# Performance work log

Hardware: AMD Instinct MI355X
Metric: run time of the kernel (lower is better)

## Reference

```python
import jax, jax.numpy as jnp
import numpy as np

NUM_NODES = 100000
NUM_EDGES = 600000
NUM_GRAPHS = 512
D = 128  # num_features == latent widths


def setup_inputs() -> dict:
    key = jax.random.key(0)
    ks = jax.random.split(key, 16)
    inp = {
        "x": jax.random.normal(ks[0], (NUM_NODES, D), dtype=jnp.float32),
        "edge_index": jax.random.randint(ks[1], (2, NUM_EDGES), 0, NUM_NODES, dtype=jnp.int32),
        "batch": jnp.sort(jax.random.randint(ks[2], (NUM_NODES,), 0, NUM_GRAPHS, dtype=jnp.int32)),
    }
    s = 1.0 / np.sqrt(D)
    # SAGEConv params per layer: lin_l (applied to mean-aggregated neighbors), lin_r (root), bias
    for i in range(3):
        inp[f"Wl{i+1}"] = jax.random.uniform(ks[3 + 3 * i], (D, D), jnp.float32, -s, s)
        inp[f"Wr{i+1}"] = jax.random.uniform(ks[4 + 3 * i], (D, D), jnp.float32, -s, s)
        inp[f"b{i+1}"] = jax.random.uniform(ks[5 + 3 * i], (D,), jnp.float32, -s, s)
    inp["Wro"] = jax.random.uniform(ks[12], (D, 1), jnp.float32, -s, s)
    inp["bro"] = jax.random.uniform(ks[13], (1,), jnp.float32, -s, s)
    return inp


def _sage_conv(h, Wl, Wr, b, src, dst):
    # mean aggregation of source features at destination nodes
    msg = jax.ops.segment_sum(h[src], dst, num_segments=NUM_NODES)          # [N, D]
    cnt = jax.ops.segment_sum(jnp.ones((src.shape[0], 1), h.dtype), dst,
                              num_segments=NUM_NODES)                        # [N, 1]
    mean = msg / jnp.maximum(cnt, 1.0)
    return mean @ Wl + h @ Wr + b


def reference(x, edge_index, batch, Wl1, Wr1, b1, Wl2, Wr2, b2, Wl3, Wr3, b3, Wro, bro):
    src, dst = edge_index[0], edge_index[1]
    h = x
    for Wl, Wr, b in ((Wl1, Wr1, b1), (Wl2, Wr2, b2), (Wl3, Wr3, b3)):
        h = jax.nn.relu(_sage_conv(h, Wl, Wr, b, src, dst))
    # per-graph sum pooling (replaces the python loop over unique batch ids)
    pooled = jax.ops.segment_sum(h, batch, num_segments=NUM_GRAPHS)  # [G, D]
    return jax.nn.sigmoid(pooled @ Wro + bro)  # [G, 1]
```

## Files before the change

### kernel.cpp

```cpp
#include <hip/hip_runtime.h>
#include <math.h>

#define N_NODES 100000
#define N_EDGES 600000
#define N_GRAPHS 512
#define D 128
#define SCAN_BS 1024
#define SCAN_NBC ((N_NODES + SCAN_BS - 1) / SCAN_BS)
#define NPART 8
#define PART_SZ (N_NODES / NPART)
#define E4 (N_EDGES / 4)
#define SPLIT_B 12500

typedef unsigned short u16;
typedef __attribute__((ext_vector_type(8))) short short8;
typedef __attribute__((ext_vector_type(4))) float f32x4;

__device__ __forceinline__ u16 f2bf(float f) {
    unsigned int u = __float_as_uint(f);
    u += 0x7FFFu + ((u >> 16) & 1u);
    return (u16)(u >> 16);
}
__device__ __forceinline__ float bf2f(u16 h) {
    return __uint_as_float(((unsigned int)h) << 16);
}
__device__ __forceinline__ void split2(float f, unsigned int& h16, unsigned int& l16) {
    unsigned int u = __float_as_uint(f);
    unsigned int hb = (u + (0x7FFFu + ((u >> 16) & 1u))) & 0xffff0000u;
    float lo = f - __uint_as_float(hb);
    unsigned int ul = __float_as_uint(lo);
    h16 = hb >> 16;
    l16 = (ul + (0x7FFFu + ((ul >> 16) & 1u))) >> 16;
}

typedef __attribute__((address_space(1))) const unsigned int gas_u32;
typedef __attribute__((address_space(3))) unsigned int las_u32;
__device__ __forceinline__ void gload16(const void* g, void* l) {
    __builtin_amdgcn_global_load_lds((gas_u32*)g, (las_u32*)l, 16, 0, 0);
}

__global__ __launch_bounds__(256) void zero_i_kernel(int* __restrict__ p, int n) {
    int i = blockIdx.x * 256 + threadIdx.x;
    if (i < n) p[i] = 0;
}

__global__ __launch_bounds__(256) void hist_kernel(const int* __restrict__ dst,
                                                   int* __restrict__ deg) {
    int e = blockIdx.x * 256 + threadIdx.x;
    if (e < N_EDGES) atomicAdd(&deg[dst[e]], 1);
}

__global__ __launch_bounds__(1024) void scan1_kernel(const int* __restrict__ deg,
                                                     int* __restrict__ excl,
                                                     int* __restrict__ blocksum) {
    __shared__ int buf[2][SCAN_BS];
    const int t = threadIdx.x;
    const int gid = blockIdx.x * SCAN_BS + t;
    int v = (gid < N_NODES) ? deg[gid] : 0;
    buf[0][t] = v;
    __syncthreads();
    int pi = 0;
    for (int off = 1; off < SCAN_BS; off <<= 1) {
        int val = buf[pi][t];
        if (t >= off) val += buf[pi][t - off];
        buf[pi ^ 1][t] = val;
        pi ^= 1;
        __syncthreads();
    }
    int incl = buf[pi][t];
    if (gid < N_NODES) excl[gid] = incl - v;
    if (t == SCAN_BS - 1) blocksum[blockIdx.x] = incl;
}

__global__ __launch_bounds__(256) void scan3_kernel(const int* __restrict__ excl,
                                                    const int* __restrict__ blocksum,
                                                    int* __restrict__ rowptr) {
    __shared__ int buf[2][128];
    const int t = threadIdx.x;
    if (t < 128) buf[0][t] = (t < SCAN_NBC) ? blocksum[t] : 0;
    __syncthreads();
    int pi = 0;
    for (int off = 1; off < 128; off <<= 1) {
        if (t < 128) {
            int val = buf[pi][t];
            if (t >= off) val += buf[pi][t - off];
            buf[pi ^ 1][t] = val;
        }
        pi ^= 1;
        __syncthreads();
    }
    const int i = blockIdx.x * 256 + t;
    if (i < N_NODES) {
        const int j = i / SCAN_BS;
        const int pref = (j == 0) ? 0 : buf[pi][j - 1];
        rowptr[i] = excl[i] + pref;
    }
    if (i == 0) rowptr[N_NODES] = N_EDGES;
}

__global__ __launch_bounds__(256) void fill_kernel(const int* __restrict__ src,
                                                   const int* __restrict__ dst,
                                                   const int* __restrict__ rowptr,
                                                   int* __restrict__ fill,
                                                   int* __restrict__ csr_src) {
    const int lo = (blockIdx.x & (NPART - 1)) * PART_SZ;
    const int i4 = (blockIdx.x >> 3) * 256 + threadIdx.x;
    if (i4 >= E4) return;
    const int4 d4 = ((const int4*)dst)[i4];
    const int4 s4 = ((const int4*)src)[i4];
    if ((unsigned)(d4.x - lo) < (unsigned)PART_SZ) {
        int pos = rowptr[d4.x] + atomicAdd(&fill[d4.x], 1);
        csr_src[pos] = s4.x;
    }
    if ((unsigned)(d4.y - lo) < (unsigned)PART_SZ) {
        int pos = rowptr[d4.y] + atomicAdd(&fill[d4.y], 1);
        csr_src[pos] = s4.y;
    }
    if ((unsigned)(d4.z - lo) < (unsigned)PART_SZ) {
        int pos = rowptr[d4.z] + atomicAdd(&fill[d4.z], 1);
        csr_src[pos] = s4.z;
    }
    if ((unsigned)(d4.w - lo) < (unsigned)PART_SZ) {
        int pos = rowptr[d4.w] + atomicAdd(&fill[d4.w], 1);
        csr_src[pos] = s4.w;
    }
}

__global__ __launch_bounds__(256) void prep_kernel(const float* __restrict__ x,
                                                   u16* __restrict__ Hhi,
                                                   u16* __restrict__ Hlo,
                                                   const float* __restrict__ Wl1, const float* __restrict__ Wr1,
                                                   const float* __restrict__ Wl2, const float* __restrict__ Wr2,
                                                   const float* __restrict__ Wl3, const float* __restrict__ Wr3,
                                                   u16* __restrict__ wph, u16* __restrict__ wpl) {
    if (blockIdx.x < SPLIT_B) {
        const int i = blockIdx.x * 256 + threadIdx.x;
        const float4 v = ((const float4*)x)[i];
        unsigned int h0, l0, h1, l1, h2, l2, h3, l3;
        split2(v.x, h0, l0); split2(v.y, h1, l1);
        split2(v.z, h2, l2); split2(v.w, h3, l3);
        uint2 oh, ol;
        oh.x = h0 | (h1 << 16); oh.y = h2 | (h3 << 16);
        ol.x = l0 | (l1 << 16); ol.y = l2 | (l3 << 16);
        ((uint2*)Hhi)[i] = oh;
        ((uint2*)Hlo)[i] = ol;
    } else {
        const int b = (blockIdx.x - SPLIT_B) * 4 + (threadIdx.x >> 6);
        const int lane = threadIdx.x & 63;
        const int layer = b >> 6;
        const int t = b & 63;
        const float* Wl = (layer == 0) ? Wl1 : (layer == 1) ? Wl2 : Wl3;
        const float* Wr = (layer == 0) ? Wr1 : (layer == 1) ? Wr2 : Wr3;
        const int nt = t >> 3, kt = t & 7;
        const int n = nt * 16 + (lane & 15);
        const int k0 = kt * 32 + (lane >> 4) * 8;
        const size_t base = (size_t)layer * 32768 + (size_t)(t * 64 + lane) * 8;
        #pragma unroll
        for (int j = 0; j < 8; ++j) {
            const int k = k0 + j;
            const float w = (k < 128) ? Wl[k * 128 + n] : Wr[(k - 128) * 128 + n];
            const u16 h = f2bf(w);
            wph[base + j] = h;
            wpl[base + j] = f2bf(w - bf2f(h));
        }
    }
}

__global__ __launch_bounds__(256) void agg_kernel(const u16* __restrict__ Hhi,
                                                  const int* __restrict__ rowptr,
                                                  const int* __restrict__ csr_src,
                                                  u16* __restrict__ Mb) {
    const int lane = threadIdx.x & 63;
    const int half = lane >> 5;
    const int q = lane & 31;
    const int node = blockIdx.x * 4 + (threadIdx.x >> 6);
    if (node >= N_NODES) return;
    const int beg = rowptr[node];
    const int end = rowptr[node + 1];
    const uint2* H64 = (const uint2*)Hhi;
    float a0 = 0.f, a1 = 0.f, a2 = 0.f, a3 = 0.f;

    for (int c0 = beg; c0 < end; c0 += 64) {
        const int nv = min(64, end - c0);
        int msrc = (c0 + lane < end) ? csr_src[c0 + lane] : 0;
        int j = 0;
        for (; j + 8 <= nv; j += 8) {
            const int t0 = __shfl(msrc, j + 0 + half);
            const int t1 = __shfl(msrc, j + 2 + half);
            const int t2 = __shfl(msrc, j + 4 + half);
            const int t3 = __shfl(msrc, j + 6 + half);
            const uint2 w0 = H64[(size_t)t0 * 32 + q];
            const uint2 w1 = H64[(size_t)t1 * 32 + q];
            const uint2 w2 = H64[(size_t)t2 * 32 + q];
            const uint2 w3 = H64[(size_t)t3 * 32 + q];
            a0 += __uint_as_float(w0.x << 16) + __uint_as_float(w1.x << 16)
                + __uint_as_float(w2.x << 16) + __uint_as_float(w3.x << 16);
            a1 += __uint_as_float(w0.x & 0xffff0000u) + __uint_as_float(w1.x & 0xffff0000u)
                + __uint_as_float(w2.x & 0xffff0000u) + __uint_as_float(w3.x & 0xffff0000u);
            a2 += __uint_as_float(w0.y << 16) + __uint_as_float(w1.y << 16)
                + __uint_as_float(w2.y << 16) + __uint_as_float(w3.y << 16);
            a3 += __uint_as_float(w0.y & 0xffff0000u) + __uint_as_float(w1.y & 0xffff0000u)
                + __uint_as_float(w2.y & 0xffff0000u) + __uint_as_float(w3.y & 0xffff0000u);
        }
        for (; j + 2 <= nv; j += 2) {
            const int s = __shfl(msrc, j + half);
            const uint2 w = H64[(size_t)s * 32 + q];
            a0 += __uint_as_float(w.x << 16);
            a1 += __uint_as_float(w.x & 0xffff0000u);
            a2 += __uint_as_float(w.y << 16);
            a3 += __uint_as_float(w.y & 0xffff0000u);
        }
        if (j < nv) {
            const int s = __shfl(msrc, j);
            if (half == 0) {
                const uint2 w = H64[(size_t)s * 32 + q];
                a0 += __uint_as_float(w.x << 16);
                a1 += __uint_as_float(w.x & 0xffff0000u);
                a2 += __uint_as_float(w.y << 16);
                a3 += __uint_as_float(w.y & 0xffff0000u);
            }
        }
    }
    a0 += __shfl_xor(a0, 32, 64);
    a1 += __shfl_xor(a1, 32, 64);
    a2 += __shfl_xor(a2, 32, 64);
    a3 += __shfl_xor(a3, 32, 64);
    if (half == 0) {
        const float inv = 1.0f / (float)max(end - beg, 1);
        uint2 o;
        o.x = (unsigned int)f2bf(a0 * inv) | ((unsigned int)f2bf(a1 * inv) << 16);
        o.y = (unsigned int)f2bf(a2 * inv) | ((unsigned int)f2bf(a3 * inv) << 16);
        ((uint2*)Mb)[(size_t)node * 32 + q] = o;
    }
}

__global__ __launch_bounds__(512, 4) void gemm_kernel(const u16* __restrict__ Mb,
                                                      const u16* Hhi, const u16* Hlo,
                                                      const u16* __restrict__ Wph,
                                                      const u16* __restrict__ Wpl,
                                                      const float* __restrict__ bias,
                                                      u16* OHhi, u16* OHlo,
                                                      const float* __restrict__ Wro,
                                                      float* rowdot) {
    __shared__ uint4 ldsAll[5120];
    const int t = threadIdx.x;
    const int lane = t & 63;
    const int wv = t >> 6;
    const int m0 = blockIdx.x * 128 + wv * 16;
    int rm = m0 + (lane & 15);
    if (rm >= N_NODES) rm = 0;
    const int ko = (lane >> 4) * 8;

    short8 am[4], ah[4], al[4];
    #pragma unroll
    for (int kt = 0; kt < 4; ++kt) {
        am[kt] = *(const short8*)(Mb  + (size_t)rm * D + kt * 32 + ko);
        ah[kt] = *(const short8*)(Hhi + (size_t)rm * D + kt * 32 + ko);
        al[kt] = *(const short8*)(Hlo + (size_t)rm * D + kt * 32 + ko);
    }

    const int cl = lane & 15;
    const int g4 = (lane >> 4) << 2;
    char* bounceB = (char*)ldsAll + 65536 + wv * 2048;

    f32x4 acc8[2][4];

#define STAGE_W(Q, B) do {                                                      \
        const uint4* gh_ = (const uint4*)Wph + (Q) * 1024;                      \
        const uint4* gl_ = (const uint4*)Wpl + (Q) * 1024;                      \
        _Pragma("unroll")                                                       \
        for (int i_ = 0; i_ < 2; ++i_) {                                        \
            gload16(gh_ + t + 512 * i_,                                         \
                    (void*)&ldsAll[(B) * 2048 + wv * 64 + 512 * i_]);           \
            gload16(gl_ + t + 512 * i_,                                         \
                    (void*)&ldsAll[(B) * 2048 + 1024 + wv * 64 + 512 * i_]);    \
        }                                                                       \
    } while (0)

#define COMPUTE_S(Q, B) do {                                                    \
        const u16* bufU_ = (const u16*)(ldsAll + (B) * 2048);                   \
        _Pragma("unroll")                                                       \
        for (int l_ = 0; l_ < 2; ++l_) {                                        \
            f32x4 acc_ = {0.f, 0.f, 0.f, 0.f};                                  \
            _Pragma("unroll")                                                   \
            for (int kt_ = 0; kt_ < 8; ++kt_) {                                 \
                const int fo_ = (l_ * 8 + kt_) * 512 + lane * 8;                \
                const short8 bh_ = *(const short8*)(bufU_ + fo_);               \
                const short8 bl_ = *(const short8*)(bufU_ + 8192 + fo_);        \
                if (kt_ < 4) {                                                  \
                    acc_ = __builtin_amdgcn_mfma_f32_16x16x32_bf16(am[kt_], bh_, acc_, 0, 0, 0); \
                    acc_ = __builtin_amdgcn_mfma_f32_16x16x32_bf16(am[kt_], bl_, acc_, 0, 0, 0); \
                } else {                                                        \
                    acc_ = __builtin_amdgcn_mfma_f32_16x16x32_bf16(ah[kt_ - 4], bh_, acc_, 0, 0, 0); \
                    acc_ = __builtin_amdgcn_mfma_f32_16x16x32_bf16(ah[kt_ - 4], bl_, acc_, 0, 0, 0); \
                    acc_ = __builtin_amdgcn_mfma_f32_16x16x32_bf16(al[kt_ - 4], bh_, acc_, 0, 0, 0); \
                }                                                               \
            }                                                                   \
            acc8[(Q) >> 1][((Q) & 1) * 2 + l_] = acc_;                          \
        }                                                                       \
    } while (0)

    STAGE_W(0, 0);
    __builtin_amdgcn_sched_barrier(0);
    STAGE_W(1, 1);
    asm volatile("s_waitcnt vmcnt(4)" ::: "memory");
    __builtin_amdgcn_s_barrier();
    COMPUTE_S(0, 0);
    __builtin_amdgcn_s_barrier();
    STAGE_W(2, 0);
    asm volatile("s_waitcnt vmcnt(4)" ::: "memory");
    __builtin_amdgcn_s_barrier();
    COMPUTE_S(1, 1);
    __builtin_amdgcn_s_barrier();
    STAGE_W(3, 1);
    asm volatile("s_waitcnt vmcnt(4)" ::: "memory");
    __builtin_amdgcn_s_barrier();
    COMPUTE_S(2, 0);
    asm volatile("s_waitcnt vmcnt(0)" ::: "memory");
    __builtin_amdgcn_s_barrier();
    COMPUTE_S(3, 1);

    if (rowdot) {
        float wsum[4] = {0.f, 0.f, 0.f, 0.f};
        #pragma unroll
        for (int si = 0; si < 2; ++si) {
            #pragma unroll
            for (int nt2 = 0; nt2 < 4; ++nt2) {
                const int col = (si * 4 + nt2) * 16 + cl;
                const float bv = bias[col];
                const float wroc = Wro[col];
                #pragma unroll
                for (int r = 0; r < 4; ++r) {
                    const float v = fmaxf(acc8[si][nt2][r] + bv, 0.f);
                    wsum[r] = fmaf(v, wroc, wsum[r]);
                }
            }
        }
        #pragma unroll
        for (int r = 0; r < 4; ++r) {
            float tsum = wsum[r];
            tsum += __shfl_down(tsum, 8, 64);
            tsum += __shfl_down(tsum, 4, 64);
            tsum += __shfl_down(tsum, 2, 64);
            tsum += __shfl_down(tsum, 1, 64);
            const int row = m0 + g4 + r;
            if (cl == 0 && row < N_NODES) {
                rowdot[row] = tsum;
            }
        }
    } else {
        #pragma unroll
        for (int si = 0; si < 2; ++si) {
            asm volatile("s_waitcnt lgkmcnt(0)" ::: "memory");
            unsigned int lo_pack[8];
            #pragma unroll
            for (int nt2 = 0; nt2 < 4; ++nt2) {
                const int col = (si * 4 + nt2) * 16 + cl;
                const float bv = bias[col];
                #pragma unroll
                for (int r = 0; r < 4; ++r) {
                    const int row16 = g4 + r;
                    const float v = fmaxf(acc8[si][nt2][r] + bv, 0.f);
                    unsigned int h16, l16;
                    split2(v, h16, l16);
                    const int boff = (row16 * 128 + (nt2 * 16 + cl) * 2) ^ ((row16 & 7) << 4);
                    *(u16*)(bounceB + boff) = (u16)h16;
                    if (r & 1) lo_pack[nt2 * 2 + (r >> 1)] |= l16 << 16;
                    else       lo_pack[nt2 * 2 + (r >> 1)]  = l16;
                }
            }
            asm volatile("s_waitcnt lgkmcnt(0)" ::: "memory");
            #pragma unroll
            for (int j = 0; j < 2; ++j) {
                const int row16 = j * 8 + (lane >> 3);
                const int blk = lane & 7;
                const uint4 vv = *(const uint4*)(bounceB + row16 * 128 + ((blk ^ (row16 & 7)) << 4));
                const int grow = blockIdx.x * 128 + wv * 16 + row16;
                if (grow < N_NODES)
                    *(uint4*)(OHhi + (size_t)grow * D + si * 64 + blk * 8) = vv;
            }
            asm volatile("s_waitcnt lgkmcnt(0)" ::: "memory");
            #pragma unroll
            for (int nt2 = 0; nt2 < 4; ++nt2) {
                #pragma unroll
                for (int r = 0; r < 4; ++r) {
                    const int row16 = g4 + r;
                    const unsigned int l16 = (lo_pack[nt2 * 2 + (r >> 1)] >> ((r & 1) * 16)) & 0xffffu;
                    const int boff = (row16 * 128 + (nt2 * 16 + cl) * 2) ^ ((row16 & 7) << 4);
                    *(u16*)(bounceB + boff) = (u16)l16;
                }
            }
            asm volatile("s_waitcnt lgkmcnt(0)" ::: "memory");
            #pragma unroll
            for (int j = 0; j < 2; ++j) {
                const int row16 = j * 8 + (lane >> 3);
                const int blk = lane & 7;
                const uint4 vv = *(const uint4*)(bounceB + row16 * 128 + ((blk ^ (row16 & 7)) << 4));
                const int grow = blockIdx.x * 128 + wv * 16 + row16;
                if (grow < N_NODES)
                    *(uint4*)(OHlo + (size_t)grow * D + si * 64 + blk * 8) = vv;
            }
        }
    }
#undef STAGE_W
#undef COMPUTE_S
}

__global__ __launch_bounds__(64) void final_kernel(const float* __restrict__ rowdot,
                                                   const int* __restrict__ batch,
                                                   const float* __restrict__ bro,
                                                   float* __restrict__ out) {
    const int g = blockIdx.x;
    const int t = threadIdx.x;
    int lo = 0, hi = N_NODES;
    while (lo < hi) { int mid = (lo + hi) >> 1; if (batch[mid] < g) lo = mid + 1; else hi = mid; }
    int lo2 = lo, hi2 = N_NODES;
    while (lo2 < hi2) { int mid = (lo2 + hi2) >> 1; if (batch[mid] < g + 1) lo2 = mid + 1; else hi2 = mid; }

    float acc = 0.0f;
    for (int i = lo + t; i < lo2; i += 64) acc += rowdot[i];
    #pragma unroll
    for (int off = 32; off > 0; off >>= 1) acc += __shfl_down(acc, off, 64);
    if (t == 0) out[g] = 1.0f / (1.0f + expf(-(acc + bro[0])));
}

extern "C" void kernel_launch(void* const* d_in, const int* in_sizes, int n_in,
                              void* d_out, int out_size, void* d_ws, size_t ws_size,
                              hipStream_t stream) {
    const float* x     = (const float*)d_in[0];
    const int*   ei    = (const int*)d_in[1];
    const int*   batch = (const int*)d_in[2];
    const int*   src   = ei;
    const int*   dst   = ei + N_EDGES;
    const float* Wl[3] = {(const float*)d_in[3], (const float*)d_in[6], (const float*)d_in[9]};
    const float* Wr[3] = {(const float*)d_in[4], (const float*)d_in[7], (const float*)d_in[10]};
    const float* bs[3] = {(const float*)d_in[5], (const float*)d_in[8], (const float*)d_in[11]};
    const float* Wro   = (const float*)d_in[12];
    const float* bro   = (const float*)d_in[13];
    float* out = (float*)d_out;

    const size_t ND = (size_t)N_NODES * D;
    char* ws = (char*)d_ws;
    u16* Hhi = (u16*)ws;
    u16* Hlo = Hhi + ND;
    u16* Mb  = Hlo + ND;
    u16* Wph = Mb + ND;
    u16* Wpl = Wph + 3 * 32768;
    int* deg      = (int*)(Wpl + 3 * 32768);
    int* fill     = deg + N_NODES;
    float* rowdot = (float*)(fill + N_NODES);
    int* excl     = (int*)(rowdot + N_NODES);
    int* blocksum = excl + N_NODES;
    int* rowptr   = blocksum + 128;
    int* csr_src  = rowptr + N_NODES + 1;

    const int EB      = (N_EDGES + 255) / 256;
    const int NB      = (N_NODES + 255) / 256;
    const int NB2     = (2 * N_NODES + 255) / 256;
    const int EPB     = ((E4 + 255) / 256) * NPART;
    const int PREP_B  = SPLIT_B + 48;
    const int AGG_B   = N_NODES / 4;
    const int GEMM_B  = (N_NODES + 127) / 128;

    zero_i_kernel<<<NB2, 256, 0, stream>>>(deg, 2 * N_NODES);
    hist_kernel<<<EB, 256, 0, stream>>>(dst, deg);
    scan1_kernel<<<SCAN_NBC, SCAN_BS, 0, stream>>>(deg, excl, blocksum);
    scan3_kernel<<<NB, 256, 0, stream>>>(excl, blocksum, rowptr);
    fill_kernel<<<EPB, 256, 0, stream>>>(src, dst, rowptr, fill, csr_src);

    prep_kernel<<<PREP_B, 256, 0, stream>>>(x, Hhi, Hlo,
                                            Wl[0], Wr[0], Wl[1], Wr[1], Wl[2], Wr[2],
                                            Wph, Wpl);

    for (int l = 0; l < 3; ++l) {
        float* rdl = (l == 2) ? rowdot : (float*)nullptr;
        agg_kernel<<<AGG_B, 256, 0, stream>>>(Hhi, rowptr, csr_src, Mb);
        gemm_kernel<<<GEMM_B, 512, 0, stream>>>(Mb, Hhi, Hlo,
                                                Wph + l * 32768, Wpl + l * 32768, bs[l],
                                                Hhi, Hlo, Wro, rdl);
    }

    final_kernel<<<N_GRAPHS, 64, 0, stream>>>(rowdot, batch, bro, out);
}
```

Measured before the change: 384.2 us.

## Process two 16-row tiles per wave in GEMM, halving block threads

The GEMM kernel now runs 4 waves of 256 threads per 128-row block, with each wave covering 32 rows as two 16-row MFMA tiles that share every B fragment read from LDS. This halves LDS reads of the weights per MFMA and interleaves two independent accumulator chains to hide MFMA latency. Weight staging now uses four loads per thread per stage, so the vmcnt waits are adjusted to match. The cost is roughly double the register use for A fragments and accumulators (launch bounds change to 256,2), which may lower occupancy.

```diff
diff --git a/kernel.cpp b/kernel.cpp
--- a/kernel.cpp
+++ b/kernel.cpp
@@ -234,7 +234,7 @@
     }
 }
 
-__global__ __launch_bounds__(512, 4) void gemm_kernel(const u16* __restrict__ Mb,
+__global__ __launch_bounds__(256, 2) void gemm_kernel(const u16* __restrict__ Mb,
                                                       const u16* Hhi, const u16* Hlo,
                                                       const u16* __restrict__ Wph,
                                                       const u16* __restrict__ Wpl,
@@ -242,38 +242,41 @@
                                                       u16* OHhi, u16* OHlo,
                                                       const float* __restrict__ Wro,
                                                       float* rowdot) {
-    __shared__ uint4 ldsAll[5120];
+    __shared__ uint4 ldsAll[4608];
     const int t = threadIdx.x;
     const int lane = t & 63;
     const int wv = t >> 6;
-    const int m0 = blockIdx.x * 128 + wv * 16;
-    int rm = m0 + (lane & 15);
-    if (rm >= N_NODES) rm = 0;
+    const int m0 = blockIdx.x * 128 + wv * 32;
+    int rm0 = m0 + (lane & 15);        if (rm0 >= N_NODES) rm0 = 0;
+    int rm1 = m0 + 16 + (lane & 15);   if (rm1 >= N_NODES) rm1 = 0;
     const int ko = (lane >> 4) * 8;
 
-    short8 am[4], ah[4], al[4];
+    short8 am0[4], ah0[4], al0[4], am1[4], ah1[4], al1[4];
     #pragma unroll
     for (int kt = 0; kt < 4; ++kt) {
-        am[kt] = *(const short8*)(Mb  + (size_t)rm * D + kt * 32 + ko);
-        ah[kt] = *(const short8*)(Hhi + (size_t)rm * D + kt * 32 + ko);
-        al[kt] = *(const short8*)(Hlo + (size_t)rm * D + kt * 32 + ko);
+        am0[kt] = *(const short8*)(Mb  + (size_t)rm0 * D + kt * 32 + ko);
+        ah0[kt] = *(const short8*)(Hhi + (size_t)rm0 * D + kt * 32 + ko);
+        al0[kt] = *(const short8*)(Hlo + (size_t)rm0 * D + kt * 32 + ko);
+        am1[kt] = *(const short8*)(Mb  + (size_t)rm1 * D + kt * 32 + ko);
+        ah1[kt] = *(const short8*)(Hhi + (size_t)rm1 * D + kt * 32 + ko);
+        al1[kt] = *(const short8*)(Hlo + (size_t)rm1 * D + kt * 32 + ko);
     }
 
     const int cl = lane & 15;
     const int g4 = (lane >> 4) << 2;
     char* bounceB = (char*)ldsAll + 65536 + wv * 2048;
 
-    f32x4 acc8[2][4];
+    f32x4 accA[2][4], accB[2][4];
 
 #define STAGE_W(Q, B) do {                                                      \
         const uint4* gh_ = (const uint4*)Wph + (Q) * 1024;                      \
         const uint4* gl_ = (const uint4*)Wpl + (Q) * 1024;                      \
         _Pragma("unroll")                                                       \
-        for (int i_ = 0; i_ < 2; ++i_) {                                        \
-            gload16(gh_ + t + 512 * i_,                                         \
-                    (void*)&ldsAll[(B) * 2048 + wv * 64 + 512 * i_]);           \
-            gload16(gl_ + t + 512 * i_,                                         \
-                    (void*)&ldsAll[(B) * 2048 + 1024 + wv * 64 + 512 * i_]);    \
+        for (int i_ = 0; i_ < 4; ++i_) {                                        \
+            gload16(gh_ + t + 256 * i_,                                         \
+                    (void*)&ldsAll[(B) * 2048 + i_ * 256 + wv * 64]);           \
+            gload16(gl_ + t + 256 * i_,                                         \
+                    (void*)&ldsAll[(B) * 2048 + 1024 + i_ * 256 + wv * 64]);    \
         }                                                                       \
     } while (0)
 
@@ -281,39 +284,46 @@
         const u16* bufU_ = (const u16*)(ldsAll + (B) * 2048);                   \
         _Pragma("unroll")                                                       \
         for (int l_ = 0; l_ < 2; ++l_) {                                        \
-            f32x4 acc_ = {0.f, 0.f, 0.f, 0.f};                                  \
+            f32x4 a0_ = {0.f, 0.f, 0.f, 0.f};                                   \
+            f32x4 a1_ = {0.f, 0.f, 0.f, 0.f};                                   \
             _Pragma("unroll")                                                   \
             for (int kt_ = 0; kt_ < 8; ++kt_) {                                 \
                 const int fo_ = (l_ * 8 + kt_) * 512 + lane * 8;                \
                 const short8 bh_ = *(const short8*)(bufU_ + fo_);               \
                 const short8 bl_ = *(const short8*)(bufU_ + 8192 + fo_);        \
                 if (kt_ < 4) {                                                  \
-                    acc_ = __builtin_amdgcn_mfma_f32_16x16x32_bf16(am[kt_], bh_, acc_, 0, 0, 0); \
-                    acc_ = __builtin_amdgcn_mfma_f32_16x16x32_bf16(am[kt_], bl_, acc_, 0, 0, 0); \
+                    a0_ = __builtin_amdgcn_mfma_f32_16x16x32_bf16(am0[kt_], bh_, a0_, 0, 0, 0); \
+                    a1_ = __builtin_amdgcn_mfma_f32_16x16x32_bf16(am1[kt_], bh_, a1_, 0, 0, 0); \
+                    a0_ = __builtin_amdgcn_mfma_f32_16x16x32_bf16(am0[kt_], bl_, a0_, 0, 0, 0); \
+                    a1_ = __builtin_amdgcn_mfma_f32_16x16x32_bf16(am1[kt_], bl_, a1_, 0, 0, 0); \
                 } else {                                                        \
-                    acc_ = __builtin_amdgcn_mfma_f32_16x16x32_bf16(ah[kt_ - 4], bh_, acc_, 0, 0, 0); \
-                    acc_ = __builtin_amdgcn_mfma_f32_16x16x32_bf16(ah[kt_ - 4], bl_, acc_, 0, 0, 0); \
-                    acc_ = __builtin_amdgcn_mfma_f32_16x16x32_bf16(al[kt_ - 4], bh_, acc_, 0, 0, 0); \
+                    a0_ = __builtin_amdgcn_mfma_f32_16x16x32_bf16(ah0[kt_ - 4], bh_, a0_, 0, 0, 0); \
+                    a1_ = __builtin_amdgcn_mfma_f32_16x16x32_bf16(ah1[kt_ - 4], bh_, a1_, 0, 0, 0); \
+                    a0_ = __builtin_amdgcn_mfma_f32_16x16x32_bf16(ah0[kt_ - 4], bl_, a0_, 0, 0, 0); \
+                    a1_ = __builtin_amdgcn_mfma_f32_16x16x32_bf16(ah1[kt_ - 4], bl_, a1_, 0, 0, 0); \
+                    a0_ = __builtin_amdgcn_mfma_f32_16x16x32_bf16(al0[kt_ - 4], bh_, a0_, 0, 0, 0); \
+                    a1_ = __builtin_amdgcn_mfma_f32_16x16x32_bf16(al1[kt_ - 4], bh_, a1_, 0, 0, 0); \
                 }                                                               \
             }                                                                   \
-            acc8[(Q) >> 1][((Q) & 1) * 2 + l_] = acc_;                          \
+            accA[(Q) >> 1][((Q) & 1) * 2 + l_] = a0_;                           \
+            accB[(Q) >> 1][((Q) & 1) * 2 + l_] = a1_;                           \
         }                                                                       \
     } while (0)
 
     STAGE_W(0, 0);
     __builtin_amdgcn_sched_barrier(0);
     STAGE_W(1, 1);
-    asm volatile("s_waitcnt vmcnt(4)" ::: "memory");
+    asm volatile("s_waitcnt vmcnt(8)" ::: "memory");
     __builtin_amdgcn_s_barrier();
     COMPUTE_S(0, 0);
     __builtin_amdgcn_s_barrier();
     STAGE_W(2, 0);
-    asm volatile("s_waitcnt vmcnt(4)" ::: "memory");
+    asm volatile("s_waitcnt vmcnt(8)" ::: "memory");
     __builtin_amdgcn_s_barrier();
     COMPUTE_S(1, 1);
     __builtin_amdgcn_s_barrier();
     STAGE_W(3, 1);
-    asm volatile("s_waitcnt vmcnt(4)" ::: "memory");
+    asm volatile("s_waitcnt vmcnt(8)" ::: "memory");
     __builtin_amdgcn_s_barrier();
     COMPUTE_S(2, 0);
     asm volatile("s_waitcnt vmcnt(0)" ::: "memory");
@@ -321,7 +331,8 @@
     COMPUTE_S(3, 1);
 
     if (rowdot) {
-        float wsum[4] = {0.f, 0.f, 0.f, 0.f};
+        float ws0[4] = {0.f, 0.f, 0.f, 0.f};
+        float ws1[4] = {0.f, 0.f, 0.f, 0.f};
         #pragma unroll
         for (int si = 0; si < 2; ++si) {
             #pragma unroll
@@ -331,74 +342,80 @@
                 const float wroc = Wro[col];
                 #pragma unroll
                 for (int r = 0; r < 4; ++r) {
-                    const float v = fmaxf(acc8[si][nt2][r] + bv, 0.f);
-                    wsum[r] = fmaf(v, wroc, wsum[r]);
+                    ws0[r] = fmaf(fmaxf(accA[si][nt2][r] + bv, 0.f), wroc, ws0[r]);
+                    ws1[r] = fmaf(fmaxf(accB[si][nt2][r] + bv, 0.f), wroc, ws1[r]);
                 }
             }
         }
         #pragma unroll
         for (int r = 0; r < 4; ++r) {
-            float tsum = wsum[r];
-            tsum += __shfl_down(tsum, 8, 64);
-            tsum += __shfl_down(tsum, 4, 64);
-            tsum += __shfl_down(tsum, 2, 64);
-            tsum += __shfl_down(tsum, 1, 64);
-            const int row = m0 + g4 + r;
-            if (cl == 0 && row < N_NODES) {
-                rowdot[row] = tsum;
+            float t0 = ws0[r], t1 = ws1[r];
+            t0 += __shfl_down(t0, 8, 64);  t1 += __shfl_down(t1, 8, 64);
+            t0 += __shfl_down(t0, 4, 64);  t1 += __shfl_down(t1, 4, 64);
+            t0 += __shfl_down(t0, 2, 64);  t1 += __shfl_down(t1, 2, 64);
+            t0 += __shfl_down(t0, 1, 64);  t1 += __shfl_down(t1, 1, 64);
+            if (cl == 0) {
+                const int row0 = m0 + g4 + r;
+                const int row1 = m0 + 16 + g4 + r;
+                if (row0 < N_NODES) rowdot[row0] = t0;
+                if (row1 < N_NODES) rowdot[row1] = t1;
             }
         }
     } else {
         #pragma unroll
         for (int si = 0; si < 2; ++si) {
-            asm volatile("s_waitcnt lgkmcnt(0)" ::: "memory");
-            unsigned int lo_pack[8];
             #pragma unroll
-            for (int nt2 = 0; nt2 < 4; ++nt2) {
-                const int col = (si * 4 + nt2) * 16 + cl;
-                const float bv = bias[col];
+            for (int p = 0; p < 2; ++p) {
+                asm volatile("s_waitcnt lgkmcnt(0)" ::: "memory");
+                unsigned int lo_pack[8];
                 #pragma unroll
-                for (int r = 0; r < 4; ++r) {
-                    const int row16 = g4 + r;
-                    const float v = fmaxf(acc8[si][nt2][r] + bv, 0.f);
-                    unsigned int h16, l16;
-                    split2(v, h16, l16);
-                    const int boff = (row16 * 128 + (nt2 * 16 + cl) * 2) ^ ((row16 & 7) << 4);
-                    *(u16*)(bounceB + boff) = (u16)h16;
-                    if (r & 1) lo_pack[nt2 * 2 + (r >> 1)] |= l16 << 16;
-                    else       lo_pack[nt2 * 2 + (r >> 1)]  = l16;
+                for (int nt2 = 0; nt2 < 4; ++nt2) {
+                    const int col = (si * 4 + nt2) * 16 + cl;
+                    const float bv = bias[col];
+                    #pragma unroll
+                    for (int r = 0; r < 4; ++r) {
+                        const int row16 = g4 + r;
+                        const f32x4 av = p ? accB[si][nt2] : accA[si][nt2];
+                        const float v = fmaxf(av[r] + bv, 0.f);
+                        unsigned int h16, l16;
+                        split2(v, h16, l16);
+                        const int boff = (row16 * 128 + (nt2 * 16 + cl) * 2) ^ ((row16 & 7) << 4);
+                        *(u16*)(bounceB + boff) = (u16)h16;
+                        if (r & 1) lo_pack[nt2 * 2 + (r >> 1)] |= l16 << 16;
+                        else       lo_pack[nt2 * 2 + (r >> 1)]  = l16;
+                    }
                 }
-            }
-            asm volatile("s_waitcnt lgkmcnt(0)" ::: "memory");
-            #pragma unroll
-            for (int j = 0; j < 2; ++j) {
-                const int row16 = j * 8 + (lane >> 3);
-                const int blk = lane & 7;
-                const uint4 vv = *(const uint4*)(bounceB + row16 * 128 + ((blk ^ (row16 & 7)) << 4));
-                const int grow = blockIdx.x * 128 + wv * 16 + row16;
-                if (grow < N_NODES)
-                    *(uint4*)(OHhi + (size_t)grow * D + si * 64 + blk * 8) = vv;
-            }
-            asm volatile("s_waitcnt lgkmcnt(0)" ::: "memory");
-            #pragma unroll
-            for (int nt2 = 0; nt2 < 4; ++nt2) {
+                asm volatile("s_waitcnt lgkmcnt(0)" ::: "memory");
                 #pragma unroll
-                for (int r = 0; r < 4; ++r) {
-                    const int row16 = g4 + r;
-                    const unsigned int l16 = (lo_pack[nt2 * 2 + (r >> 1)] >> ((r & 1) * 16)) & 0xffffu;
-                    const int boff = (row16 * 128 + (nt2 * 16 + cl) * 2) ^ ((row16 & 7) << 4);
-                    *(u16*)(bounceB + boff) = (u16)l16;
+                for (int j = 0; j < 2; ++j) {
+                    const int row16 = j * 8 + (lane >> 3);
+                    const int blk = lane & 7;
+                    const uint4 vv = *(const uint4*)(bounceB + row16 * 128 + ((blk ^ (row16 & 7)) << 4));
+                    const int grow = m0 + p * 16 + row16;
+                    if (grow < N_NODES)
+                        *(uint4*)(OHhi + (size_t)grow * D + si * 64 + blk * 8) = vv;
                 }
-            }
-            asm volatile("s_waitcnt lgkmcnt(0)" ::: "memory");
-            #pragma unroll
-            for (int j = 0; j < 2; ++j) {
-                const int row16 = j * 8 + (lane >> 3);
-                const int blk = lane & 7;
-                const uint4 vv = *(const uint4*)(bounceB + row16 * 128 + ((blk ^ (row16 & 7)) << 4));
-                const int grow = blockIdx.x * 128 + wv * 16 + row16;
-                if (grow < N_NODES)
-                    *(uint4*)(OHlo + (size_t)grow * D + si * 64 + blk * 8) = vv;
+                asm volatile("s_waitcnt lgkmcnt(0)" ::: "memory");
+                #pragma unroll
+                for (int nt2 = 0; nt2 < 4; ++nt2) {
+                    #pragma unroll
+                    for (int r = 0; r < 4; ++r) {
+                        const int row16 = g4 + r;
+                        const unsigned int l16 = (lo_pack[nt2 * 2 + (r >> 1)] >> ((r & 1) * 16)) & 0xffffu;
+                        const int boff = (row16 * 128 + (nt2 * 16 + cl) * 2) ^ ((row16 & 7) << 4);
+                        *(u16*)(bounceB + boff) = (u16)l16;
+                    }
+                }
+                asm volatile("s_waitcnt lgkmcnt(0)" ::: "memory");
+                #pragma unroll
+                for (int j = 0; j < 2; ++j) {
+                    const int row16 = j * 8 + (lane >> 3);
+                    const int blk = lane & 7;
+                    const uint4 vv = *(const uint4*)(bounceB + row16 * 128 + ((blk ^ (row16 & 7)) << 4));
+                    const int grow = m0 + p * 16 + row16;
+                    if (grow < N_NODES)
+                        *(uint4*)(OHlo + (size_t)grow * D + si * 64 + blk * 8) = vv;
+                }
             }
         }
     }
@@ -475,7 +492,7 @@
     for (int l = 0; l < 3; ++l) {
         float* rdl = (l == 2) ? rowdot : (float*)nullptr;
         agg_kernel<<<AGG_B, 256, 0, stream>>>(Hhi, rowptr, csr_src, Mb);
-        gemm_kernel<<<GEMM_B, 512, 0, stream>>>(Mb, Hhi, Hlo,
+        gemm_kernel<<<GEMM_B, 256, 0, stream>>>(Mb, Hhi, Hlo,
                                                 Wph + l * 32768, Wpl + l * 32768, bs[l],
                                                 Hhi, Hlo, Wro, rdl);
     }
```

New measurement: 392.4 us. 1.02x slower.

## Fuse neighbor mean aggregation into GEMM kernel with ping-pong feature buffers

Applied to the files above, without the earlier changes.

Removes the separate agg_kernel and performs the CSR mean gather inside the GEMM kernel's A-operand load, with each lane walking its own row's neighbor list and accumulating 8 bf16 values per k-tile. Activations now ping-pong between two buffers so the fused kernel does not overwrite rows other blocks still read. This drops three launches and the Mb round-trip through memory. In exchange the gather is per-row serial with divergent degrees across the wave, 16-byte scattered loads and a lower parallelism pattern than the dedicated wave-per-node aggregation, plus extra register pressure in a 512-thread GEMM.

```diff
diff --git a/kernel.cpp b/kernel.cpp
--- a/kernel.cpp
+++ b/kernel.cpp
@@ -166,80 +166,15 @@
     }
 }
 
-__global__ __launch_bounds__(256) void agg_kernel(const u16* __restrict__ Hhi,
-                                                  const int* __restrict__ rowptr,
-                                                  const int* __restrict__ csr_src,
-                                                  u16* __restrict__ Mb) {
-    const int lane = threadIdx.x & 63;
-    const int half = lane >> 5;
-    const int q = lane & 31;
-    const int node = blockIdx.x * 4 + (threadIdx.x >> 6);
-    if (node >= N_NODES) return;
-    const int beg = rowptr[node];
-    const int end = rowptr[node + 1];
-    const uint2* H64 = (const uint2*)Hhi;
-    float a0 = 0.f, a1 = 0.f, a2 = 0.f, a3 = 0.f;
-
-    for (int c0 = beg; c0 < end; c0 += 64) {
-        const int nv = min(64, end - c0);
-        int msrc = (c0 + lane < end) ? csr_src[c0 + lane] : 0;
-        int j = 0;
-        for (; j + 8 <= nv; j += 8) {
-            const int t0 = __shfl(msrc, j + 0 + half);
-            const int t1 = __shfl(msrc, j + 2 + half);
-            const int t2 = __shfl(msrc, j + 4 + half);
-            const int t3 = __shfl(msrc, j + 6 + half);
-            const uint2 w0 = H64[(size_t)t0 * 32 + q];
-            const uint2 w1 = H64[(size_t)t1 * 32 + q];
-            const uint2 w2 = H64[(size_t)t2 * 32 + q];
-            const uint2 w3 = H64[(size_t)t3 * 32 + q];
-            a0 += __uint_as_float(w0.x << 16) + __uint_as_float(w1.x << 16)
-                + __uint_as_float(w2.x << 16) + __uint_as_float(w3.x << 16);
-            a1 += __uint_as_float(w0.x & 0xffff0000u) + __uint_as_float(w1.x & 0xffff0000u)
-                + __uint_as_float(w2.x & 0xffff0000u) + __uint_as_float(w3.x & 0xffff0000u);
-            a2 += __uint_as_float(w0.y << 16) + __uint_as_float(w1.y << 16)
-                + __uint_as_float(w2.y << 16) + __uint_as_float(w3.y << 16);
-            a3 += __uint_as_float(w0.y & 0xffff0000u) + __uint_as_float(w1.y & 0xffff0000u)
-                + __uint_as_float(w2.y & 0xffff0000u) + __uint_as_float(w3.y & 0xffff0000u);
-        }
-        for (; j + 2 <= nv; j += 2) {
-            const int s = __shfl(msrc, j + half);
-            const uint2 w = H64[(size_t)s * 32 + q];
-            a0 += __uint_as_float(w.x << 16);
-            a1 += __uint_as_float(w.x & 0xffff0000u);
-            a2 += __uint_as_float(w.y << 16);
-            a3 += __uint_as_float(w.y & 0xffff0000u);
-        }
-        if (j < nv) {
-            const int s = __shfl(msrc, j);
-            if (half == 0) {
-                const uint2 w = H64[(size_t)s * 32 + q];
-                a0 += __uint_as_float(w.x << 16);
-                a1 += __uint_as_float(w.x & 0xffff0000u);
-                a2 += __uint_as_float(w.y << 16);
-                a3 += __uint_as_float(w.y & 0xffff0000u);
-            }
-        }
-    }
-    a0 += __shfl_xor(a0, 32, 64);
-    a1 += __shfl_xor(a1, 32, 64);
-    a2 += __shfl_xor(a2, 32, 64);
-    a3 += __shfl_xor(a3, 32, 64);
-    if (half == 0) {
-        const float inv = 1.0f / (float)max(end - beg, 1);
-        uint2 o;
-        o.x = (unsigned int)f2bf(a0 * inv) | ((unsigned int)f2bf(a1 * inv) << 16);
-        o.y = (unsigned int)f2bf(a2 * inv) | ((unsigned int)f2bf(a3 * inv) << 16);
-        ((uint2*)Mb)[(size_t)node * 32 + q] = o;
-    }
-}
-
-__global__ __launch_bounds__(512, 4) void gemm_kernel(const u16* __restrict__ Mb,
-                                                      const u16* Hhi, const u16* Hlo,
+__global__ __launch_bounds__(512, 4) void gemm_kernel(const u16* __restrict__ INhi,
+                                                      const u16* __restrict__ INlo,
+                                                      const int* __restrict__ rowptr,
+                                                      const int* __restrict__ csr_src,
                                                       const u16* __restrict__ Wph,
                                                       const u16* __restrict__ Wpl,
                                                       const float* __restrict__ bias,
-                                                      u16* OHhi, u16* OHlo,
+                                                      u16* __restrict__ OHhi,
+                                                      u16* __restrict__ OHlo,
                                                       const float* __restrict__ Wro,
                                                       float* rowdot) {
     __shared__ uint4 ldsAll[5120];
@@ -247,16 +182,60 @@
     const int lane = t & 63;
     const int wv = t >> 6;
     const int m0 = blockIdx.x * 128 + wv * 16;
-    int rm = m0 + (lane & 15);
-    if (rm >= N_NODES) rm = 0;
+    const int row16 = m0 + (lane & 15);
+    int rm = row16; if (rm >= N_NODES) rm = 0;
     const int ko = (lane >> 4) * 8;
 
-    short8 am[4], ah[4], al[4];
+    int beg = 0, deg = 0;
+    if (row16 < N_NODES) {
+        beg = rowptr[row16];
+        deg = rowptr[row16 + 1] - beg;
+    }
+    float ac[4][8];
     #pragma unroll
     for (int kt = 0; kt < 4; ++kt) {
-        am[kt] = *(const short8*)(Mb  + (size_t)rm * D + kt * 32 + ko);
-        ah[kt] = *(const short8*)(Hhi + (size_t)rm * D + kt * 32 + ko);
-        al[kt] = *(const short8*)(Hlo + (size_t)rm * D + kt * 32 + ko);
+        #pragma unroll
+        for (int j = 0; j < 8; ++j) ac[kt][j] = 0.f;
+    }
+    int s_cur = (deg > 0) ? csr_src[beg] : 0;
+    for (int n = 0; __any(n < deg); ++n) {
+        const bool act = n < deg;
+        const int s_nxt = (n + 1 < deg) ? csr_src[beg + n + 1] : 0;
+        if (act) {
+            const size_t rb = (size_t)s_cur * D + ko;
+            #pragma unroll
+            for (int kt = 0; kt < 4; ++kt) {
+                const uint4 v = *(const uint4*)(INhi + rb + kt * 32);
+                ac[kt][0] += __uint_as_float(v.x << 16);
+                ac[kt][1] += __uint_as_float(v.x & 0xffff0000u);
+                ac[kt][2] += __uint_as_float(v.y << 16);
+                ac[kt][3] += __uint_as_float(v.y & 0xffff0000u);
+                ac[kt][4] += __uint_as_float(v.z << 16);
+                ac[kt][5] += __uint_as_float(v.z & 0xffff0000u);
+                ac[kt][6] += __uint_as_float(v.w << 16);
+                ac[kt][7] += __uint_as_float(v.w & 0xffff0000u);
+            }
+        }
+        s_cur = s_nxt;
+    }
+    const float inv = 1.0f / (float)max(deg, 1);
+    short8 am[4];
+    #pragma unroll
+    for (int kt = 0; kt < 4; ++kt) {
+        uint4 u;
+        u.x = (unsigned)f2bf(ac[kt][0] * inv) | ((unsigned)f2bf(ac[kt][1] * inv) << 16);
+        u.y = (unsigned)f2bf(ac[kt][2] * inv) | ((unsigned)f2bf(ac[kt][3] * inv) << 16);
+        u.z = (unsigned)f2bf(ac[kt][4] * inv) | ((unsigned)f2bf(ac[kt][5] * inv) << 16);
+        u.w = (unsigned)f2bf(ac[kt][6] * inv) | ((unsigned)f2bf(ac[kt][7] * inv) << 16);
+        am[kt] = __builtin_bit_cast(short8, u);
+    }
+    __builtin_amdgcn_sched_barrier(0);
+
+    short8 ah[4], al[4];
+    #pragma unroll
+    for (int kt = 0; kt < 4; ++kt) {
+        ah[kt] = *(const short8*)(INhi + (size_t)rm * D + kt * 32 + ko);
+        al[kt] = *(const short8*)(INlo + (size_t)rm * D + kt * 32 + ko);
     }
 
     const int cl = lane & 15;
@@ -359,11 +338,11 @@
                 const float bv = bias[col];
                 #pragma unroll
                 for (int r = 0; r < 4; ++r) {
-                    const int row16 = g4 + r;
+                    const int rr = g4 + r;
                     const float v = fmaxf(acc8[si][nt2][r] + bv, 0.f);
                     unsigned int h16, l16;
                     split2(v, h16, l16);
-                    const int boff = (row16 * 128 + (nt2 * 16 + cl) * 2) ^ ((row16 & 7) << 4);
+                    const int boff = (rr * 128 + (nt2 * 16 + cl) * 2) ^ ((rr & 7) << 4);
                     *(u16*)(bounceB + boff) = (u16)h16;
                     if (r & 1) lo_pack[nt2 * 2 + (r >> 1)] |= l16 << 16;
                     else       lo_pack[nt2 * 2 + (r >> 1)]  = l16;
@@ -372,10 +351,10 @@
             asm volatile("s_waitcnt lgkmcnt(0)" ::: "memory");
             #pragma unroll
             for (int j = 0; j < 2; ++j) {
-                const int row16 = j * 8 + (lane >> 3);
+                const int rr = j * 8 + (lane >> 3);
                 const int blk = lane & 7;
-                const uint4 vv = *(const uint4*)(bounceB + row16 * 128 + ((blk ^ (row16 & 7)) << 4));
-                const int grow = blockIdx.x * 128 + wv * 16 + row16;
+                const uint4 vv = *(const uint4*)(bounceB + rr * 128 + ((blk ^ (rr & 7)) << 4));
+                const int grow = m0 + rr;
                 if (grow < N_NODES)
                     *(uint4*)(OHhi + (size_t)grow * D + si * 64 + blk * 8) = vv;
             }
@@ -384,19 +363,19 @@
             for (int nt2 = 0; nt2 < 4; ++nt2) {
                 #pragma unroll
                 for (int r = 0; r < 4; ++r) {
-                    const int row16 = g4 + r;
+                    const int rr = g4 + r;
                     const unsigned int l16 = (lo_pack[nt2 * 2 + (r >> 1)] >> ((r & 1) * 16)) & 0xffffu;
-                    const int boff = (row16 * 128 + (nt2 * 16 + cl) * 2) ^ ((row16 & 7) << 4);
+                    const int boff = (rr * 128 + (nt2 * 16 + cl) * 2) ^ ((rr & 7) << 4);
                     *(u16*)(bounceB + boff) = (u16)l16;
                 }
             }
             asm volatile("s_waitcnt lgkmcnt(0)" ::: "memory");
             #pragma unroll
             for (int j = 0; j < 2; ++j) {
-                const int row16 = j * 8 + (lane >> 3);
+                const int rr = j * 8 + (lane >> 3);
                 const int blk = lane & 7;
-                const uint4 vv = *(const uint4*)(bounceB + row16 * 128 + ((blk ^ (row16 & 7)) << 4));
-                const int grow = blockIdx.x * 128 + wv * 16 + row16;
+                const uint4 vv = *(const uint4*)(bounceB + rr * 128 + ((blk ^ (rr & 7)) << 4));
+                const int grow = m0 + rr;
                 if (grow < N_NODES)
                     *(uint4*)(OHlo + (size_t)grow * D + si * 64 + blk * 8) = vv;
             }
@@ -441,10 +420,11 @@
 
     const size_t ND = (size_t)N_NODES * D;
     char* ws = (char*)d_ws;
-    u16* Hhi = (u16*)ws;
-    u16* Hlo = Hhi + ND;
-    u16* Mb  = Hlo + ND;
-    u16* Wph = Mb + ND;
+    u16* Ahi = (u16*)ws;
+    u16* Alo = Ahi + ND;
+    u16* Bhi = Alo + ND;
+    u16* Blo = Bhi + ND;
+    u16* Wph = Blo + ND;
     u16* Wpl = Wph + 3 * 32768;
     int* deg      = (int*)(Wpl + 3 * 32768);
     int* fill     = deg + N_NODES;
@@ -459,7 +439,6 @@
     const int NB2     = (2 * N_NODES + 255) / 256;
     const int EPB     = ((E4 + 255) / 256) * NPART;
     const int PREP_B  = SPLIT_B + 48;
-    const int AGG_B   = N_NODES / 4;
     const int GEMM_B  = (N_NODES + 127) / 128;
 
     zero_i_kernel<<<NB2, 256, 0, stream>>>(deg, 2 * N_NODES);
@@ -468,17 +447,19 @@
     scan3_kernel<<<NB, 256, 0, stream>>>(excl, blocksum, rowptr);
     fill_kernel<<<EPB, 256, 0, stream>>>(src, dst, rowptr, fill, csr_src);
 
-    prep_kernel<<<PREP_B, 256, 0, stream>>>(x, Hhi, Hlo,
+    prep_kernel<<<PREP_B, 256, 0, stream>>>(x, Ahi, Alo,
                                             Wl[0], Wr[0], Wl[1], Wr[1], Wl[2], Wr[2],
                                             Wph, Wpl);
 
-    for (int l = 0; l < 3; ++l) {
-        float* rdl = (l == 2) ? rowdot : (float*)nullptr;
-        agg_kernel<<<AGG_B, 256, 0, stream>>>(Hhi, rowptr, csr_src, Mb);
-        gemm_kernel<<<GEMM_B, 512, 0, stream>>>(Mb, Hhi, Hlo,
-                                                Wph + l * 32768, Wpl + l * 32768, bs[l],
-                                                Hhi, Hlo, Wro, rdl);
-    }
+    gemm_kernel<<<GEMM_B, 512, 0, stream>>>(Ahi, Alo, rowptr, csr_src,
+                                            Wph, Wpl, bs[0],
+                                            Bhi, Blo, Wro, (float*)nullptr);
+    gemm_kernel<<<GEMM_B, 512, 0, stream>>>(Bhi, Blo, rowptr, csr_src,
+                                            Wph + 32768, Wpl + 32768, bs[1],
+                                            Ahi, Alo, Wro, (float*)nullptr);
+    gemm_kernel<<<GEMM_B, 512, 0, stream>>>(Ahi, Alo, rowptr, csr_src,
+                                            Wph + 2 * 32768, Wpl + 2 * 32768, bs[2],
+                                            Bhi, Blo, Wro, rowdot);
 
     final_kernel<<<N_GRAPHS, 64, 0, stream>>>(rowdot, batch, bro, out);
 }
```

Result: faster. 362.0 us (-5.8%).
